# Optimization experiments

Hardware: AMD Instinct MI355X
Metric: run time of the kernel (lower is better)

The kernel has to match this reference:

```python
import jax, jax.numpy as jnp
import numpy as np

N_EMBD = 1024
N_HEAD = 16
HEAD_DIM = N_EMBD // N_HEAD


def setup_inputs() -> dict:
    key = jax.random.key(0)
    kx, kq, kk, kv, ko = jax.random.split(key, 5)
    s = 1.0 / np.sqrt(N_EMBD)
    return {
        "x": jax.random.normal(kx, (4, 2048, N_EMBD), dtype=jnp.float32),
        "Wq": jax.random.normal(kq, (N_EMBD, N_EMBD), dtype=jnp.float32) * s,
        "Wk": jax.random.normal(kk, (N_EMBD, N_EMBD), dtype=jnp.float32) * s,
        "Wv": jax.random.normal(kv, (N_EMBD, N_EMBD), dtype=jnp.float32) * s,
        "Wo": jax.random.normal(ko, (N_EMBD, N_EMBD), dtype=jnp.float32) * s,
    }


def reference(x, Wq, Wk, Wv, Wo):
    B, T, C = x.shape
    H, D = N_HEAD, HEAD_DIM
    # projections; torch Linear computes x @ W.T
    q = (x @ Wq.T).reshape(B, T, H, D).transpose(0, 2, 1, 3)  # [B,H,T,D]
    k = (x @ Wk.T).reshape(B, T, H, D).transpose(0, 2, 1, 3)
    v = (x @ Wv.T).reshape(B, T, H, D).transpose(0, 2, 1, 3)
    scores = jnp.einsum("bhtd,bhsd->bhts", q, k) / np.sqrt(D).astype(np.float32)
    causal = jnp.tril(jnp.ones((T, T), dtype=bool))
    scores = jnp.where(causal, scores, -jnp.inf)
    attn = jax.nn.softmax(scores, axis=-1)
    out = jnp.einsum("bhts,bhsd->bhtd", attn, v)  # [B,H,T,D]
    out = out.transpose(0, 2, 1, 3).reshape(B, T, C)
    return out @ Wo.T
```

## Files before the change

### kernel.cpp

```cpp
#include <hip/hip_runtime.h>
#include <hip/hip_bf16.h>


typedef __bf16 bf16_t;
typedef __bf16 bf16x4 __attribute__((ext_vector_type(4)));
typedef __bf16 bf16x8 __attribute__((ext_vector_type(8)));
typedef float  f32x4  __attribute__((ext_vector_type(4)));

#define MFMA16(a, b, c) __builtin_amdgcn_mfma_f32_16x16x32_bf16(a, b, c, 0, 0, 0)

__device__ __forceinline__ float exp2_(float x) {
#if __has_builtin(__builtin_amdgcn_exp2f)
    return __builtin_amdgcn_exp2f(x);
#else
    return __expf(x * 0.6931471805599453f);
#endif
}

__device__ __forceinline__ void gload_lds16(const bf16_t* g, bf16_t* l) {
    __builtin_amdgcn_global_load_lds(
        (const __attribute__((address_space(1))) void*)g,
        (__attribute__((address_space(3))) void*)l, 16, 0, 0);
}

__global__ __launch_bounds__(256)
void cast_f32_bf16(const float* __restrict__ in, bf16_t* __restrict__ out, int n8) {
    int i = blockIdx.x * 256 + threadIdx.x;
    if (i >= n8) return;
    const float4* p = (const float4*)in;
    float4 a = p[i * 2], b = p[i * 2 + 1];
    bf16x8 o;
    o[0] = (bf16_t)a.x; o[1] = (bf16_t)a.y; o[2] = (bf16_t)a.z; o[3] = (bf16_t)a.w;
    o[4] = (bf16_t)b.x; o[5] = (bf16_t)b.y; o[6] = (bf16_t)b.z; o[7] = (bf16_t)b.w;
    *(bf16x8*)(out + (size_t)i * 8) = o;
}

__global__ __launch_bounds__(256)
void cast4_f32_bf16(const float* __restrict__ i0, const float* __restrict__ i1,
                    const float* __restrict__ i2, const float* __restrict__ i3,
                    bf16_t* o0, bf16_t* o1, bf16_t* o2, bf16_t* o3, int n8) {
    const float* in = blockIdx.y == 0 ? i0 : blockIdx.y == 1 ? i1 : blockIdx.y == 2 ? i2 : i3;
    bf16_t*     out = blockIdx.y == 0 ? o0 : blockIdx.y == 1 ? o1 : blockIdx.y == 2 ? o2 : o3;
    int i = blockIdx.x * 256 + threadIdx.x;
    if (i >= n8) return;
    const float4* p = (const float4*)in;
    float4 a = p[i * 2], b = p[i * 2 + 1];
    bf16x8 o;
    o[0] = (bf16_t)a.x; o[1] = (bf16_t)a.y; o[2] = (bf16_t)a.z; o[3] = (bf16_t)a.w;
    o[4] = (bf16_t)b.x; o[5] = (bf16_t)b.y; o[6] = (bf16_t)b.z; o[7] = (bf16_t)b.w;
    *(bf16x8*)(out + (size_t)i * 8) = o;
}

template<int OUT_BF16>
__global__ __launch_bounds__(256)
void gemm_bt(const bf16_t* __restrict__ A, const bf16_t* __restrict__ B,
             void* __restrict__ Cv, int M, int N, int K) {
    __shared__ bf16_t As[128 * 32];
    __shared__ bf16_t Bs[128 * 32];
    const int tid = threadIdx.x;
    const int lane = tid & 63;
    const int w = tid >> 6;
    const int wm = w >> 1, wn = w & 1;
    const int g = lane >> 4, c = lane & 15;
    const long bm = (long)blockIdx.x * 128;
    const long bn = (long)blockIdx.y * 128;

    f32x4 acc[4][4] = {};

    const int srow = tid >> 2;
    const int scol = (tid & 3) << 3;
    const bf16_t* Ag = A + (bm + srow) * (long)K + scol;
    const bf16_t* Bg = B + (bn + srow) * (long)K + scol;
    bf16_t* AsW = As + tid * 8;
    bf16_t* BsW = Bs + tid * 8;

    for (int k0 = 0; k0 < K; k0 += 32) {
        gload_lds16(Ag + k0,                 AsW);
        gload_lds16(Ag + k0 + (long)64 * K,  AsW + 2048);
        gload_lds16(Bg + k0,                 BsW);
        gload_lds16(Bg + k0 + (long)64 * K,  BsW + 2048);
        __syncthreads();
        bf16x8 af[4], bfr[4];
        #pragma unroll
        for (int m = 0; m < 4; ++m)
            af[m] = *(const bf16x8*)(As + (wm * 64 + m * 16 + c) * 32 + g * 8);
        #pragma unroll
        for (int n = 0; n < 4; ++n)
            bfr[n] = *(const bf16x8*)(Bs + (wn * 64 + n * 16 + c) * 32 + g * 8);
        #pragma unroll
        for (int m = 0; m < 4; ++m)
            #pragma unroll
            for (int n = 0; n < 4; ++n)
                acc[m][n] = MFMA16(af[m], bfr[n], acc[m][n]);
        __syncthreads();
    }
    #pragma unroll
    for (int m = 0; m < 4; ++m)
        #pragma unroll
        for (int n = 0; n < 4; ++n)
            #pragma unroll
            for (int i = 0; i < 4; ++i) {
                long row = bm + wm * 64 + m * 16 + g * 4 + i;
                long col = bn + wn * 64 + n * 16 + c;
                float v = acc[m][n][i];
                if (OUT_BF16) ((bf16_t*)Cv)[row * N + col] = (bf16_t)v;
                else          ((float*)Cv)[row * N + col]  = v;
            }
}


__device__ __forceinline__ void stage_K(const bf16_t* Kp, long rowb, int kb, int hcol,
                                        bf16_t* Kbuf, int tid) {
    #pragma unroll
    for (int i = 0; i < 2; ++i) {
        int row = i * 32 + (tid >> 3);
        int lb  = (tid & 7) ^ (row & 7);
        gload_lds16(Kp + (rowb + kb + row) * 3072 + hcol + lb * 8,
                    Kbuf + i * 2048 + tid * 8);
    }
}

__device__ __forceinline__ void load_V(const bf16_t* Vp, long rowb, int kb, int hcol,
                                       int tid, unsigned int* vr) {
    const int d0 = (tid & 31) * 2;
    const int k0 = (tid >> 5) * 8;
    const unsigned int* src =
        (const unsigned int*)(Vp + (rowb + kb + k0) * 3072 + hcol + d0);
    #pragma unroll
    for (int i = 0; i < 8; ++i) vr[i] = src[(size_t)i * 1536];
}

__device__ __forceinline__ void write_Vt(bf16_t* Vbuf, int tid, const unsigned int* vr) {
    const int d0 = (tid & 31) * 2;
    const int k0 = (tid >> 5) * 8;
    unsigned int lo[4], hi[4];
    #pragma unroll
    for (int i = 0; i < 4; ++i) {
        lo[i] = (vr[2 * i] & 0xffffu) | (vr[2 * i + 1] << 16);
        hi[i] = (vr[2 * i] >> 16)     | (vr[2 * i + 1] & 0xffff0000u);
    }
    *(uint4*)&Vbuf[(d0 + 0) * 72 + k0] = make_uint4(lo[0], lo[1], lo[2], lo[3]);
    *(uint4*)&Vbuf[(d0 + 1) * 72 + k0] = make_uint4(hi[0], hi[1], hi[2], hi[3]);
}

__global__ __launch_bounds__(256)
void attn_kernel(const bf16_t* __restrict__ Qp, const bf16_t* __restrict__ Kp,
                 const bf16_t* __restrict__ Vp, bf16_t* __restrict__ O) {
    __shared__ bf16_t Ks[2][64 * 64];
    __shared__ bf16_t Vts[2][64 * 72];
    __shared__ bf16_t PW[4][32 * 72];

    const int tid = threadIdx.x, lane = tid & 63, w = tid >> 6;
    const int g = lane >> 4, c = lane & 15;
    const int bh = blockIdx.x, bx = blockIdx.y;
    const int b = bh >> 4, h = bh & 15;
    const long rowb = (long)b * 2048;
    const int hcol = h * 64;
    const float QSCL = 0.18033688011112042f;

    for (int pass = 0; pass < 2; ++pass) {
        const int q0  = pass ? (15 - bx) : bx;
        const int qlo = q0 * 128 + w * 32;
        const int nkt = 2 * q0 + 2;

        bf16x8 qf[2][2];
        #pragma unroll
        for (int m = 0; m < 2; ++m)
            #pragma unroll
            for (int ks = 0; ks < 2; ++ks) {
                qf[m][ks] = *(const bf16x8*)(Qp + (rowb + qlo + m * 16 + c) * 3072 +
                                             hcol + ks * 32 + g * 8);
                #pragma unroll
                for (int j = 0; j < 8; ++j)
                    qf[m][ks][j] = (bf16_t)((float)qf[m][ks][j] * QSCL);
            }

        float m_r[2] = {-1e30f, -1e30f};
        float l_r[2] = {0.f, 0.f};
        f32x4 acc[2][4] = {};

        stage_K(Kp, rowb, 0, hcol, Ks[0], tid);
        {
            unsigned int vr0[8];
            load_V(Vp, rowb, 0, hcol, tid, vr0);
            write_Vt(Vts[0], tid, vr0);
        }
        __syncthreads();

        for (int t = 0; t < nkt; ++t) {
            const int cur = t & 1;
            const int kb = t * 64;
            const bool pre = (t + 1 < nkt);
            unsigned int vr[8];
            if (pre) {
                stage_K(Kp, rowb, kb + 64, hcol, Ks[cur ^ 1], tid);
                load_V(Vp, rowb, kb + 64, hcol, tid, vr);
            }

            if (kb <= qlo + 31) {
                f32x4 sacc[2][4] = {};
                #pragma unroll
                for (int nt = 0; nt < 4; ++nt) {
                    const int row = nt * 16 + c;
                    #pragma unroll
                    for (int ks = 0; ks < 2; ++ks) {
                        bf16x8 kf = *(const bf16x8*)&Ks[cur][row * 64 +
                                        (((ks * 4 + g) ^ (c & 7)) * 8)];
                        sacc[0][nt] = MFMA16(kf, qf[0][ks], sacc[0][nt]);
                        sacc[1][nt] = MFMA16(kf, qf[1][ks], sacc[1][nt]);
                    }
                }
                if (kb + 63 > qlo) {
                    #pragma unroll
                    for (int m = 0; m < 2; ++m) {
                        const int q = qlo + m * 16 + c;
                        #pragma unroll
                        for (int nt = 0; nt < 4; ++nt)
                            #pragma unroll
                            for (int i = 0; i < 4; ++i) {
                                int key = kb + nt * 16 + g * 4 + i;
                                if (key > q) sacc[m][nt][i] = -1e30f;
                            }
                    }
                }

                float scl[2];
                #pragma unroll
                for (int m = 0; m < 2; ++m) {
                    float mx = sacc[m][0][0];
                    #pragma unroll
                    for (int nt = 0; nt < 4; ++nt)
                        #pragma unroll
                        for (int i = 0; i < 4; ++i)
                            mx = fmaxf(mx, sacc[m][nt][i]);
                    mx = fmaxf(mx, __shfl_xor(mx, 16, 64));
                    mx = fmaxf(mx, __shfl_xor(mx, 32, 64));
                    float mnew = fmaxf(m_r[m], mx);
                    scl[m] = exp2_(m_r[m] - mnew);
                    m_r[m] = mnew;
                    float rs = 0.f;
                    #pragma unroll
                    for (int nt = 0; nt < 4; ++nt)
                        #pragma unroll
                        for (int i = 0; i < 4; ++i) {
                            float pv = exp2_(sacc[m][nt][i] - mnew);
                            sacc[m][nt][i] = pv;
                            rs += pv;
                        }
                    rs += __shfl_xor(rs, 16, 64);
                    rs += __shfl_xor(rs, 32, 64);
                    l_r[m] = l_r[m] * scl[m] + rs;
                    #pragma unroll
                    for (int nt = 0; nt < 4; ++nt) {
                        bf16x4 t4;
                        #pragma unroll
                        for (int i = 0; i < 4; ++i) t4[i] = (bf16_t)sacc[m][nt][i];
                        *(bf16x4*)&PW[w][(m * 16 + c) * 72 + nt * 16 + g * 4] = t4;
                    }
                }
                #pragma unroll
                for (int m = 0; m < 2; ++m)
                    #pragma unroll
                    for (int nt = 0; nt < 4; ++nt)
                        acc[m][nt] *= scl[m];

                #pragma unroll
                for (int ks = 0; ks < 2; ++ks) {
                    bf16x8 pf0 = *(const bf16x8*)&PW[w][(c)      * 72 + ks * 32 + g * 8];
                    bf16x8 pf1 = *(const bf16x8*)&PW[w][(16 + c) * 72 + ks * 32 + g * 8];
                    #pragma unroll
                    for (int nt = 0; nt < 4; ++nt) {
                        bf16x8 vf = *(const bf16x8*)&Vts[cur][(nt * 16 + c) * 72 +
                                                              ks * 32 + g * 8];
                        acc[0][nt] = MFMA16(vf, pf0, acc[0][nt]);
                        acc[1][nt] = MFMA16(vf, pf1, acc[1][nt]);
                    }
                }
            }

            if (pre) write_Vt(Vts[cur ^ 1], tid, vr);
            __syncthreads();
        }

        #pragma unroll
        for (int m = 0; m < 2; ++m) {
            float rl = __builtin_amdgcn_rcpf(l_r[m]);
            #pragma unroll
            for (int nt = 0; nt < 4; ++nt) {
                bf16x4 t4;
                #pragma unroll
                for (int i = 0; i < 4; ++i) t4[i] = (bf16_t)(acc[m][nt][i] * rl);
                *(bf16x4*)&PW[w][(m * 16 + c) * 72 + nt * 16 + g * 4] = t4;
            }
        }
        #pragma unroll
        for (int r0 = 0; r0 < 4; ++r0) {
            int row = r0 * 8 + (lane >> 3);
            int ch  = (lane & 7) * 8;
            bf16x8 v = *(const bf16x8*)&PW[w][row * 72 + ch];
            *(bf16x8*)&O[(rowb + qlo + row) * 1024 + hcol + ch] = v;
        }
    }
}

extern "C" void kernel_launch(void* const* d_in, const int* in_sizes, int n_in,
                              void* d_out, int out_size, void* d_ws, size_t ws_size,
                              hipStream_t stream) {
    const float* x  = (const float*)d_in[0];
    const float* Wq = (const float*)d_in[1];
    const float* Wk = (const float*)d_in[2];
    const float* Wv = (const float*)d_in[3];
    const float* Wo = (const float*)d_in[4];

    const int M = 8192;
    const int C = 1024;

    char* ws = (char*)d_ws;
    bf16_t* xb   = (bf16_t*)(ws);
    bf16_t* wqkv = (bf16_t*)(ws + ((size_t)16 << 20));
    bf16_t* wob  = (bf16_t*)(ws + ((size_t)22 << 20));
    bf16_t* qkv  = (bf16_t*)(ws + ((size_t)24 << 20));
    bf16_t* aob  = (bf16_t*)(ws + ((size_t)72 << 20));

    cast_f32_bf16<<<(M * C / 8) / 256, 256, 0, stream>>>(x, xb, M * C / 8);
    cast4_f32_bf16<<<dim3((C * C / 8) / 256, 4), 256, 0, stream>>>(
        Wq, Wk, Wv, Wo,
        wqkv, wqkv + (size_t)(C * C), wqkv + (size_t)(2 * C * C), wob, C * C / 8);

    gemm_bt<1><<<dim3(M / 128, 3072 / 128), 256, 0, stream>>>(xb, wqkv, qkv, M, 3072, C);

    attn_kernel<<<dim3(64, 8), 256, 0, stream>>>(
        qkv, qkv + 1024, qkv + 2048, aob);

    gemm_bt<0><<<dim3(M / 128, C / 128), 256, 0, stream>>>(aob, wob, d_out, M, C, C);
}
```

Before: 194.0 us.

## Split attention work across 8 waves of 16 rows and add lazy rescaling

The attention kernel moves from 256 threads, where each wave owns 32 query rows, to 512 threads, where each wave owns 16 rows. This halves per-wave register state and the per-thread K/V staging load, and it raises the number of waves sharing each K/V tile. It also adds a lazy online-softmax rescale that only rescales acc and l when the running max grows by more than 8 (log2 units). The trade-off is that each K/V fragment read from LDS now feeds half as many MFMAs, and more waves take part in each __syncthreads barrier.

```diff
diff --git a/kernel.cpp b/kernel.cpp
--- a/kernel.cpp
+++ b/kernel.cpp
@@ -111,44 +111,40 @@
 
 __device__ __forceinline__ void stage_K(const bf16_t* Kp, long rowb, int kb, int hcol,
                                         bf16_t* Kbuf, int tid) {
-    #pragma unroll
-    for (int i = 0; i < 2; ++i) {
-        int row = i * 32 + (tid >> 3);
-        int lb  = (tid & 7) ^ (row & 7);
-        gload_lds16(Kp + (rowb + kb + row) * 3072 + hcol + lb * 8,
-                    Kbuf + i * 2048 + tid * 8);
-    }
+    int row = tid >> 3;
+    int lb  = (tid & 7) ^ (row & 7);
+    gload_lds16(Kp + (rowb + kb + row) * 3072 + hcol + lb * 8, Kbuf + tid * 8);
 }
 
 __device__ __forceinline__ void load_V(const bf16_t* Vp, long rowb, int kb, int hcol,
                                        int tid, unsigned int* vr) {
     const int d0 = (tid & 31) * 2;
-    const int k0 = (tid >> 5) * 8;
+    const int k0 = (tid >> 5) * 4;
     const unsigned int* src =
         (const unsigned int*)(Vp + (rowb + kb + k0) * 3072 + hcol + d0);
     #pragma unroll
-    for (int i = 0; i < 8; ++i) vr[i] = src[(size_t)i * 1536];
+    for (int i = 0; i < 4; ++i) vr[i] = src[(size_t)i * 1536];
 }
 
 __device__ __forceinline__ void write_Vt(bf16_t* Vbuf, int tid, const unsigned int* vr) {
     const int d0 = (tid & 31) * 2;
-    const int k0 = (tid >> 5) * 8;
-    unsigned int lo[4], hi[4];
+    const int k0 = (tid >> 5) * 4;
+    unsigned int lo[2], hi[2];
     #pragma unroll
-    for (int i = 0; i < 4; ++i) {
+    for (int i = 0; i < 2; ++i) {
         lo[i] = (vr[2 * i] & 0xffffu) | (vr[2 * i + 1] << 16);
         hi[i] = (vr[2 * i] >> 16)     | (vr[2 * i + 1] & 0xffff0000u);
     }
-    *(uint4*)&Vbuf[(d0 + 0) * 72 + k0] = make_uint4(lo[0], lo[1], lo[2], lo[3]);
-    *(uint4*)&Vbuf[(d0 + 1) * 72 + k0] = make_uint4(hi[0], hi[1], hi[2], hi[3]);
-}
-
-__global__ __launch_bounds__(256)
+    *(uint2*)&Vbuf[(d0 + 0) * 72 + k0] = make_uint2(lo[0], lo[1]);
+    *(uint2*)&Vbuf[(d0 + 1) * 72 + k0] = make_uint2(hi[0], hi[1]);
+}
+
+__global__ __launch_bounds__(512, 4)
 void attn_kernel(const bf16_t* __restrict__ Qp, const bf16_t* __restrict__ Kp,
                  const bf16_t* __restrict__ Vp, bf16_t* __restrict__ O) {
     __shared__ bf16_t Ks[2][64 * 64];
     __shared__ bf16_t Vts[2][64 * 72];
-    __shared__ bf16_t PW[4][32 * 72];
+    __shared__ bf16_t PW[8][16 * 72];
 
     const int tid = threadIdx.x, lane = tid & 63, w = tid >> 6;
     const int g = lane >> 4, c = lane & 15;
@@ -160,28 +156,25 @@
 
     for (int pass = 0; pass < 2; ++pass) {
         const int q0  = pass ? (15 - bx) : bx;
-        const int qlo = q0 * 128 + w * 32;
+        const int qlo = q0 * 128 + w * 16;
         const int nkt = 2 * q0 + 2;
 
-        bf16x8 qf[2][2];
-        #pragma unroll
-        for (int m = 0; m < 2; ++m)
+        bf16x8 qf[2];
+        #pragma unroll
+        for (int ks = 0; ks < 2; ++ks) {
+            qf[ks] = *(const bf16x8*)(Qp + (rowb + qlo + c) * 3072 +
+                                      hcol + ks * 32 + g * 8);
             #pragma unroll
-            for (int ks = 0; ks < 2; ++ks) {
-                qf[m][ks] = *(const bf16x8*)(Qp + (rowb + qlo + m * 16 + c) * 3072 +
-                                             hcol + ks * 32 + g * 8);
-                #pragma unroll
-                for (int j = 0; j < 8; ++j)
-                    qf[m][ks][j] = (bf16_t)((float)qf[m][ks][j] * QSCL);
-            }
-
-        float m_r[2] = {-1e30f, -1e30f};
-        float l_r[2] = {0.f, 0.f};
-        f32x4 acc[2][4] = {};
+            for (int j = 0; j < 8; ++j)
+                qf[ks][j] = (bf16_t)((float)qf[ks][j] * QSCL);
+        }
+
+        float m_r = -1e30f, l_r = 0.f;
+        f32x4 acc[4] = {};
 
         stage_K(Kp, rowb, 0, hcol, Ks[0], tid);
         {
-            unsigned int vr0[8];
+            unsigned int vr0[4];
             load_V(Vp, rowb, 0, hcol, tid, vr0);
             write_Vt(Vts[0], tid, vr0);
         }
@@ -191,14 +184,14 @@
             const int cur = t & 1;
             const int kb = t * 64;
             const bool pre = (t + 1 < nkt);
-            unsigned int vr[8];
+            unsigned int vr[4];
             if (pre) {
                 stage_K(Kp, rowb, kb + 64, hcol, Ks[cur ^ 1], tid);
                 load_V(Vp, rowb, kb + 64, hcol, tid, vr);
             }
 
-            if (kb <= qlo + 31) {
-                f32x4 sacc[2][4] = {};
+            if (kb <= qlo + 15) {
+                f32x4 sacc[4] = {};
                 #pragma unroll
                 for (int nt = 0; nt < 4; ++nt) {
                     const int row = nt * 16 + c;
@@ -206,74 +199,66 @@
                     for (int ks = 0; ks < 2; ++ks) {
                         bf16x8 kf = *(const bf16x8*)&Ks[cur][row * 64 +
                                         (((ks * 4 + g) ^ (c & 7)) * 8)];
-                        sacc[0][nt] = MFMA16(kf, qf[0][ks], sacc[0][nt]);
-                        sacc[1][nt] = MFMA16(kf, qf[1][ks], sacc[1][nt]);
+                        sacc[nt] = MFMA16(kf, qf[ks], sacc[nt]);
                     }
                 }
                 if (kb + 63 > qlo) {
-                    #pragma unroll
-                    for (int m = 0; m < 2; ++m) {
-                        const int q = qlo + m * 16 + c;
-                        #pragma unroll
-                        for (int nt = 0; nt < 4; ++nt)
-                            #pragma unroll
-                            for (int i = 0; i < 4; ++i) {
-                                int key = kb + nt * 16 + g * 4 + i;
-                                if (key > q) sacc[m][nt][i] = -1e30f;
-                            }
-                    }
-                }
-
-                float scl[2];
-                #pragma unroll
-                for (int m = 0; m < 2; ++m) {
-                    float mx = sacc[m][0][0];
-                    #pragma unroll
-                    for (int nt = 0; nt < 4; ++nt)
-                        #pragma unroll
-                        for (int i = 0; i < 4; ++i)
-                            mx = fmaxf(mx, sacc[m][nt][i]);
-                    mx = fmaxf(mx, __shfl_xor(mx, 16, 64));
-                    mx = fmaxf(mx, __shfl_xor(mx, 32, 64));
-                    float mnew = fmaxf(m_r[m], mx);
-                    scl[m] = exp2_(m_r[m] - mnew);
-                    m_r[m] = mnew;
-                    float rs = 0.f;
+                    const int q = qlo + c;
                     #pragma unroll
                     for (int nt = 0; nt < 4; ++nt)
                         #pragma unroll
                         for (int i = 0; i < 4; ++i) {
-                            float pv = exp2_(sacc[m][nt][i] - mnew);
-                            sacc[m][nt][i] = pv;
-                            rs += pv;
+                            int key = kb + nt * 16 + g * 4 + i;
+                            if (key > q) sacc[nt][i] = -1e30f;
                         }
-                    rs += __shfl_xor(rs, 16, 64);
-                    rs += __shfl_xor(rs, 32, 64);
-                    l_r[m] = l_r[m] * scl[m] + rs;
-                    #pragma unroll
-                    for (int nt = 0; nt < 4; ++nt) {
-                        bf16x4 t4;
-                        #pragma unroll
-                        for (int i = 0; i < 4; ++i) t4[i] = (bf16_t)sacc[m][nt][i];
-                        *(bf16x4*)&PW[w][(m * 16 + c) * 72 + nt * 16 + g * 4] = t4;
+                }
+
+                float mx = sacc[0][0];
+                #pragma unroll
+                for (int nt = 0; nt < 4; ++nt)
+                    #pragma unroll
+                    for (int i = 0; i < 4; ++i)
+                        mx = fmaxf(mx, sacc[nt][i]);
+                mx = fmaxf(mx, __shfl_xor(mx, 16, 64));
+                mx = fmaxf(mx, __shfl_xor(mx, 32, 64));
+                if (__any(mx > m_r + 8.f)) {
+                    float mnew = fmaxf(m_r, mx);
+                    float scl = exp2_(m_r - mnew);
+                    #pragma unroll
+                    for (int nt = 0; nt < 4; ++nt)
+                        acc[nt] *= scl;
+                    l_r *= scl;
+                    m_r = mnew;
+                }
+                float rs = 0.f;
+                #pragma unroll
+                for (int nt = 0; nt < 4; ++nt)
+                    #pragma unroll
+                    for (int i = 0; i < 4; ++i) {
+                        float pv = exp2_(sacc[nt][i] - m_r);
+                        sacc[nt][i] = pv;
+                        rs += pv;
                     }
-                }
-                #pragma unroll
-                for (int m = 0; m < 2; ++m)
-                    #pragma unroll
-                    for (int nt = 0; nt < 4; ++nt)
-                        acc[m][nt] *= scl[m];
+                rs += __shfl_xor(rs, 16, 64);
+                rs += __shfl_xor(rs, 32, 64);
+                l_r += rs;
+
+                #pragma unroll
+                for (int nt = 0; nt < 4; ++nt) {
+                    bf16x4 t4;
+                    #pragma unroll
+                    for (int i = 0; i < 4; ++i) t4[i] = (bf16_t)sacc[nt][i];
+                    *(bf16x4*)&PW[w][c * 72 + nt * 16 + g * 4] = t4;
+                }
 
                 #pragma unroll
                 for (int ks = 0; ks < 2; ++ks) {
-                    bf16x8 pf0 = *(const bf16x8*)&PW[w][(c)      * 72 + ks * 32 + g * 8];
-                    bf16x8 pf1 = *(const bf16x8*)&PW[w][(16 + c) * 72 + ks * 32 + g * 8];
+                    bf16x8 pf = *(const bf16x8*)&PW[w][c * 72 + ks * 32 + g * 8];
                     #pragma unroll
                     for (int nt = 0; nt < 4; ++nt) {
                         bf16x8 vf = *(const bf16x8*)&Vts[cur][(nt * 16 + c) * 72 +
                                                               ks * 32 + g * 8];
-                        acc[0][nt] = MFMA16(vf, pf0, acc[0][nt]);
-                        acc[1][nt] = MFMA16(vf, pf1, acc[1][nt]);
+                        acc[nt] = MFMA16(vf, pf, acc[nt]);
                     }
                 }
             }
@@ -282,20 +267,19 @@
             __syncthreads();
         }
 
-        #pragma unroll
-        for (int m = 0; m < 2; ++m) {
-            float rl = __builtin_amdgcn_rcpf(l_r[m]);
+        {
+            float rl = __builtin_amdgcn_rcpf(l_r);
             #pragma unroll
             for (int nt = 0; nt < 4; ++nt) {
                 bf16x4 t4;
                 #pragma unroll
-                for (int i = 0; i < 4; ++i) t4[i] = (bf16_t)(acc[m][nt][i] * rl);
-                *(bf16x4*)&PW[w][(m * 16 + c) * 72 + nt * 16 + g * 4] = t4;
+                for (int i = 0; i < 4; ++i) t4[i] = (bf16_t)(acc[nt][i] * rl);
+                *(bf16x4*)&PW[w][c * 72 + nt * 16 + g * 4] = t4;
             }
         }
         #pragma unroll
-        for (int r0 = 0; r0 < 4; ++r0) {
-            int row = r0 * 8 + (lane >> 3);
+        for (int p = 0; p < 2; ++p) {
+            int row = p * 8 + (lane >> 3);
             int ch  = (lane & 7) * 8;
             bf16x8 v = *(const bf16x8*)&PW[w][row * 72 + ch];
             *(bf16x8*)&O[(rowb + qlo + row) * 1024 + hcol + ch] = v;
@@ -329,7 +313,7 @@
 
     gemm_bt<1><<<dim3(M / 128, 3072 / 128), 256, 0, stream>>>(xb, wqkv, qkv, M, 3072, C);
 
-    attn_kernel<<<dim3(64, 8), 256, 0, stream>>>(
+    attn_kernel<<<dim3(64, 8), 512, 0, stream>>>(
         qkv, qkv + 1024, qkv + 2048, aob);
 
     gemm_bt<0><<<dim3(M / 128, C / 128), 256, 0, stream>>>(aob, wob, d_out, M, C, C);
```

Result: faster. 187.9 us (-3.1%).
